# Kernel tuning notes

Hardware: AMD Instinct MI355X
Metric: run time of the kernel (lower is better)

The kernel has to match this reference:

```python
import jax, jax.numpy as jnp
import numpy as np

B = 1024
NUM_DENSE = 13
NUM_SPARSE = 26
VOCAB = 100000
EMB_DIM = 16
BOT = [512, 256, 64, 16]
TOP = [1024, 512, 256]
D_INT = BOT[-1] + NUM_SPARSE * EMB_DIM  # 432
OUT_INT = D_INT * (D_INT + 1) // 2      # 93528


def setup_inputs() -> dict:
    key = jax.random.key(0)
    ks = jax.random.split(key, 32)
    inp = {
        "dense_features": jax.random.normal(ks[0], (B, NUM_DENSE), jnp.float32),
        "sparse_features": jax.random.randint(ks[1], (B, NUM_SPARSE), 0, VOCAB),
        "emb_tables": jax.random.normal(ks[2], (NUM_SPARSE, VOCAB, EMB_DIM), jnp.float32) * 0.02,
    }
    # bottom MLP weights (in, out) convention
    dims = [NUM_DENSE] + BOT
    for i in range(len(BOT)):
        inp[f"bw{i}"] = jax.random.normal(ks[3 + i], (dims[i], dims[i + 1]), jnp.float32) * 0.02
        inp[f"bb{i}"] = jnp.zeros((dims[i + 1],), jnp.float32)
    tdims = [BOT[-1] + OUT_INT] + TOP + [1]
    for i in range(len(TOP) + 1):
        inp[f"tw{i}"] = jax.random.normal(ks[10 + i], (tdims[i], tdims[i + 1]), jnp.float32) * 0.02
        inp[f"tb{i}"] = jnp.zeros((tdims[i + 1],), jnp.float32)
    return inp


def _forward(dense_features, emb_tables, bws, bbs, tws, tbs, sparse_features):
    # bottom MLP: Linear+ReLU stacks
    h = dense_features
    for w, b in zip(bws, bbs):
        h = jax.nn.relu(h @ w + b)
    dense_out = h  # (B, 16)
    # embedding lookups: table t indexed by column t of sparse_features
    # emb_tables: (F, V, E); gather per-table then flatten -> (B, F*E)
    emb = jnp.take_along_axis(
        emb_tables[None],  # (1, F, V, E)
        sparse_features.T[None, :, :, None].transpose(0, 1, 2, 3) * 0 + sparse_features.T[None, :, :, None],
        axis=2,
    )  # placeholder avoided below
    # cleaner: vmap over tables
    emb = jax.vmap(lambda tbl, idx: tbl[idx], in_axes=(0, 1))(emb_tables, sparse_features)  # (F, B, E)
    emb = jnp.transpose(emb, (1, 0, 2)).reshape(dense_features.shape[0], -1)  # (B, F*E)
    x = jnp.concatenate([dense_out, emb], axis=1)  # (B, D_INT)
    # pairwise interaction: upper triangle (incl. diagonal) of outer product.
    iu0, iu1 = np.triu_indices(x.shape[1])
    inter = x[:, iu0] * x[:, iu1]  # (B, OUT_INT) -- only needed entries
    z = jnp.concatenate([dense_out, inter], axis=1)
    n_top = len(tws)
    for i, (w, b) in enumerate(zip(tws, tbs)):
        z = z @ w + b
        if i < n_top - 1:
            z = jax.nn.relu(z)
    return z


def reference(dense_features, sparse_features, emb_tables,
              bw0, bb0, bw1, bb1, bw2, bb2, bw3, bb3,
              tw0, tb0, tw1, tb1, tw2, tb2, tw3, tb3):
    bws = [bw0, bw1, bw2, bw3]
    bbs = [bb0, bb1, bb2, bb3]
    tws = [tw0, tw1, tw2, tw3]
    tbs = [tb0, tb1, tb2, tb3]
    return _forward(dense_features, emb_tables, bws, bbs, tws, tbs, sparse_features)
```

## Files before the change

### kernel.cpp

```cpp
#include <hip/hip_runtime.h>
#include <stdint.h>

typedef unsigned short ushort_t;
typedef __attribute__((ext_vector_type(4))) float f32x4;
typedef __attribute__((ext_vector_type(8))) short s16x8;

#define DEVFN static __device__ __forceinline__

constexpr int B_   = 1024;
constexpr int P_   = 93528;
constexpr int K1   = 93544;
constexpr int Kp   = 94208;
constexpr int SPLITS = 16;
constexpr int KCH  = Kp / SPLITS;
constexpr int KSTEPS = KCH / 64;

DEVFN ushort_t f2bf(float f) {
  union { float f; unsigned int u; } x; x.f = f;
  unsigned int r = x.u + 0x7FFFu + ((x.u >> 16) & 1u);
  return (ushort_t)(r >> 16);
}

DEVFN void gload_lds16(const void* g, void* l) {
  __builtin_amdgcn_global_load_lds((const __attribute__((address_space(1))) unsigned int*)g,
                                   (__attribute__((address_space(3))) unsigned int*)l, 16, 0, 0);
}

__global__ __launch_bounds__(256) void k_pre(const float* __restrict__ dense,
    const int* __restrict__ sparse, const float* __restrict__ tbl,
    const float* __restrict__ bw0, const float* __restrict__ bb0,
    const float* __restrict__ bw1, const float* __restrict__ bb1,
    const float* __restrict__ bw2, const float* __restrict__ bb2,
    const float* __restrict__ bw3, const float* __restrict__ bb3,
    const float* __restrict__ tw0,
    int* __restrict__ iu, float* __restrict__ xT, ushort_t* __restrict__ WT) {
  __shared__ float sm[3392];
  int bid = blockIdx.x, t = threadIdx.x;
  if (bid < 256) {
    float* xs = sm;
    float* h1 = sm + 64;
    float* h2 = h1 + 2048;
    float* h3 = h2 + 1024;
    int m0 = bid * 4;
    if (t < 52) xs[t] = dense[m0 * 13 + t];
    __syncthreads();
    #pragma unroll
    for (int h = 0; h < 2; ++h) {
      int n = h * 256 + t;
      float a[4];
      float bv = bb0[n];
      #pragma unroll
      for (int r = 0; r < 4; ++r) a[r] = bv;
      for (int k = 0; k < 13; ++k) {
        float w = bw0[k * 512 + n];
        #pragma unroll
        for (int r = 0; r < 4; ++r) a[r] = fmaf(xs[r * 13 + k], w, a[r]);
      }
      #pragma unroll
      for (int r = 0; r < 4; ++r) h1[r * 512 + n] = fmaxf(a[r], 0.f);
    }
    __syncthreads();
    {
      int n = t;
      float a[4];
      float bv = bb1[n];
      #pragma unroll
      for (int r = 0; r < 4; ++r) a[r] = bv;
      #pragma unroll 8
      for (int k = 0; k < 512; ++k) {
        float w = bw1[k * 256 + n];
        #pragma unroll
        for (int r = 0; r < 4; ++r) a[r] = fmaf(h1[r * 512 + k], w, a[r]);
      }
      #pragma unroll
      for (int r = 0; r < 4; ++r) h2[r * 256 + n] = fmaxf(a[r], 0.f);
    }
    __syncthreads();
    {
      int n = t & 63, r = t >> 6;
      float a = bb2[n];
      #pragma unroll 8
      for (int k = 0; k < 256; ++k) a = fmaf(h2[r * 256 + k], bw2[k * 64 + n], a);
      h3[r * 64 + n] = fmaxf(a, 0.f);
    }
    __syncthreads();
    if (t < 64) {
      int n = t & 15, r = t >> 4;
      float a = bb3[n];
      #pragma unroll 8
      for (int k = 0; k < 64; ++k) a = fmaf(h3[r * 64 + k], bw3[k * 16 + n], a);
      xT[(size_t)n * B_ + m0 + r] = fmaxf(a, 0.f);
    }
  } else if (bid < 624) {
    int bb = bid - 256;
    int k = bb * 256 + t;
    if (bb < 8) {
      int idx = bb * 256 + t;
      xT[432 * 1024 + idx] = (idx < 1024) ? 1.f : 0.f;
    }
    if (k >= Kp) return;
    int v;
    if (k < 16) v = k | (432 << 16);
    else if (k >= K1) v = 433 | (433 << 16);
    else {
      int p = k - 16;
      float s = sqrtf((float)(748225 - 8 * p));
      int i = (int)((865.0f - s) * 0.5f);
      if (i < 0) i = 0; if (i > 431) i = 431;
      while (i < 431 && (i + 1) * (865 - (i + 1)) / 2 <= p) ++i;
      while (i > 0 && i * (865 - i) / 2 > p) --i;
      int j = i + (p - i * (865 - i) / 2);
      v = i | (j << 16);
    }
    iu[k] = v;
  } else if (bid < 728) {
    int e = bid - 624;
    int f = e >> 2;
    int b = (e & 3) * 256 + t;
    int idx = sparse[(size_t)b * 26 + f];
    const float4* src = (const float4*)(tbl + ((size_t)f * 100000 + idx) * 16);
    #pragma unroll
    for (int q = 0; q < 4; ++q) {
      float4 v = src[q];
      int r = 16 + f * 16 + q * 4;
      xT[(size_t)(r + 0) * B_ + b] = v.x;
      xT[(size_t)(r + 1) * B_ + b] = v.y;
      xT[(size_t)(r + 2) * B_ + b] = v.z;
      xT[(size_t)(r + 3) * B_ + b] = v.w;
    }
  } else {
    int idx = bid - 728;
    int k0 = (idx % 368) * 256, n0 = (idx / 368) * 64;
    int nl = t & 63, kq = t >> 6;
    int n = n0 + nl;
    int kbase = k0 + kq * 64;
    const float* src = tw0 + (size_t)kbase * 1024 + n;
    ushort_t* dst = WT + ((size_t)(kbase >> 3) * 1024 + n) * 8;
    bool full = (kbase + 64 <= K1);
    #pragma unroll
    for (int g = 0; g < 8; ++g) {
      float v[8];
      if (full) {
        #pragma unroll
        for (int e = 0; e < 8; ++e) v[e] = src[(size_t)(g * 8 + e) << 10];
      } else {
        #pragma unroll
        for (int e = 0; e < 8; ++e) {
          int k = kbase + g * 8 + e;
          v[e] = (k < K1) ? src[(size_t)(g * 8 + e) << 10] : 0.f;
        }
      }
      union { uint32_t w4[4]; int4 v4; } o;
      asm("v_cvt_pk_bf16_f32 %0, %1, %2" : "=v"(o.w4[0]) : "v"(v[0]), "v"(v[1]));
      asm("v_cvt_pk_bf16_f32 %0, %1, %2" : "=v"(o.w4[1]) : "v"(v[2]), "v"(v[3]));
      asm("v_cvt_pk_bf16_f32 %0, %1, %2" : "=v"(o.w4[2]) : "v"(v[4]), "v"(v[5]));
      asm("v_cvt_pk_bf16_f32 %0, %1, %2" : "=v"(o.w4[3]) : "v"(v[6]), "v"(v[7]));
      *(int4*)(dst + (size_t)g * 8192) = o.v4;
    }
  }
}

__global__ __launch_bounds__(256, 8) void k_genz(const float* __restrict__ xT,
                                                 const int* __restrict__ iu,
                                                 ushort_t* __restrict__ Z) {
  __shared__ int ls_iu[512];
  int idx = blockIdx.x, t = threadIdx.x;
  int l = t & 63, w = t >> 6;
  int mb = (idx & 15) * 64;
  int kt = (idx >> 4) * 512;
  ls_iu[t] = iu[kt + t];
  ls_iu[256 + t] = iu[kt + 256 + t];
  __syncthreads();
  uint32_t moff = mb + l;
  int kw = w * 128;
  #pragma unroll 2
  for (int g = 0; g < 16; ++g) {
    int kloc = kw + g * 8;
    int4 ij0 = *(const int4*)&ls_iu[kloc];
    int4 ij1 = *(const int4*)&ls_iu[kloc + 4];
    float p[8];
    {
      int v0 = ij0.x, v1 = ij0.y, v2 = ij0.z, v3 = ij0.w;
      p[0] = xT[(uint32_t)((v0 & 0xFFFF) << 10) + moff] * xT[(uint32_t)((v0 >> 16) << 10) + moff];
      p[1] = xT[(uint32_t)((v1 & 0xFFFF) << 10) + moff] * xT[(uint32_t)((v1 >> 16) << 10) + moff];
      p[2] = xT[(uint32_t)((v2 & 0xFFFF) << 10) + moff] * xT[(uint32_t)((v2 >> 16) << 10) + moff];
      p[3] = xT[(uint32_t)((v3 & 0xFFFF) << 10) + moff] * xT[(uint32_t)((v3 >> 16) << 10) + moff];
      v0 = ij1.x; v1 = ij1.y; v2 = ij1.z; v3 = ij1.w;
      p[4] = xT[(uint32_t)((v0 & 0xFFFF) << 10) + moff] * xT[(uint32_t)((v0 >> 16) << 10) + moff];
      p[5] = xT[(uint32_t)((v1 & 0xFFFF) << 10) + moff] * xT[(uint32_t)((v1 >> 16) << 10) + moff];
      p[6] = xT[(uint32_t)((v2 & 0xFFFF) << 10) + moff] * xT[(uint32_t)((v2 >> 16) << 10) + moff];
      p[7] = xT[(uint32_t)((v3 & 0xFFFF) << 10) + moff] * xT[(uint32_t)((v3 >> 16) << 10) + moff];
    }
    union { uint32_t w4[4]; int4 v4; } o;
    asm("v_cvt_pk_bf16_f32 %0, %1, %2" : "=v"(o.w4[0]) : "v"(p[0]), "v"(p[1]));
    asm("v_cvt_pk_bf16_f32 %0, %1, %2" : "=v"(o.w4[1]) : "v"(p[2]), "v"(p[3]));
    asm("v_cvt_pk_bf16_f32 %0, %1, %2" : "=v"(o.w4[2]) : "v"(p[4]), "v"(p[5]));
    asm("v_cvt_pk_bf16_f32 %0, %1, %2" : "=v"(o.w4[3]) : "v"(p[6]), "v"(p[7]));
    int kglob = kt + kloc;
    *(int4*)&Z[((size_t)(kglob >> 3) * 1024 + moff) * 8] = o.v4;
  }
}

__global__ __launch_bounds__(512, 2) void k_gemm(const ushort_t* __restrict__ Z,
                                                 const ushort_t* __restrict__ WT,
                                                 float* __restrict__ part) {
  __shared__ ushort_t lds[65536];
  int t = threadIdx.x;
  int bid = blockIdx.x;
  int x = bid & 7, r = bid >> 3;
  int g = (x << 3) | (r & 7);
  int s = g >> 2;
  int m0 = (g & 3) * 256, n0 = (r >> 3) * 256;
  int kb = s * KCH;

  int rr = t >> 3, cc = t & 7;
  int cs = cc ^ (rr & 7);
  const ushort_t* pa0 = Z  + (((size_t)(kb >> 3) + cs) * 1024 + m0 + rr) * 8;
  const ushort_t* pb0 = WT + (((size_t)(kb >> 3) + cs) * 1024 + n0 + rr) * 8;
  int l0 = t * 8;

  int w = t >> 6, l = t & 63;
  int wm = (w >> 2) * 128, wn = (w & 3) * 64;
  int lhi = l >> 4, llo = l & 15;

  f32x4 acc[8][4];
  #pragma unroll
  for (int a = 0; a < 8; ++a)
    #pragma unroll
    for (int b = 0; b < 4; ++b) acc[a][b] = f32x4{0.f, 0.f, 0.f, 0.f};

  s16x8 bf[4][2], afX[4], afY[4];

  auto rdA = [&](s16x8* dst, int mfb, const ushort_t* Ab) {
    #pragma unroll
    for (int j = 0; j < 2; ++j)
      #pragma unroll
      for (int ks = 0; ks < 2; ++ks) {
        int row = wm + (mfb + j) * 16 + llo;
        int ch = (ks * 4 + lhi) ^ (row & 7);
        dst[j * 2 + ks] = *(const s16x8*)&Ab[row * 64 + ch * 8];
      }
  };
  auto rdB = [&](const ushort_t* Bb) {
    #pragma unroll
    for (int nf = 0; nf < 4; ++nf)
      #pragma unroll
      for (int ks = 0; ks < 2; ++ks) {
        int row = wn + nf * 16 + llo;
        int ch = (ks * 4 + lhi) ^ (row & 7);
        bf[nf][ks] = *(const s16x8*)&Bb[row * 64 + ch * 8];
      }
  };

#define MFMA_PHASE(P, AF)                                                        \
  __builtin_amdgcn_s_barrier();                                                  \
  asm volatile("s_waitcnt lgkmcnt(0)" ::: "memory");                             \
  __builtin_amdgcn_sched_barrier(0);                                             \
  __builtin_amdgcn_s_setprio(1);                                                 \
  _Pragma("unroll")                                                              \
  for (int j = 0; j < 2; ++j)                                                    \
    _Pragma("unroll")                                                            \
    for (int nf = 0; nf < 4; ++nf)                                               \
      _Pragma("unroll")                                                          \
      for (int ks = 0; ks < 2; ++ks)                                             \
        acc[(P) * 2 + j][nf] = __builtin_amdgcn_mfma_f32_16x16x32_bf16(          \
            AF[j * 2 + ks], bf[nf][ks], acc[(P) * 2 + j][nf], 0, 0, 0);          \
  __builtin_amdgcn_s_setprio(0);                                                 \
  __builtin_amdgcn_sched_barrier(0);                                             \
  __builtin_amdgcn_s_barrier();

  #pragma unroll
  for (int i = 0; i < 4; ++i) gload_lds16(pa0 + i * 512, &lds[i * 4096 + l0]);
  #pragma unroll
  for (int i = 0; i < 4; ++i) gload_lds16(pb0 + i * 512, &lds[32768 + i * 4096 + l0]);
  #pragma unroll
  for (int i = 0; i < 4; ++i) gload_lds16(pb0 + 65536 + i * 512, &lds[32768 + 16384 + i * 4096 + l0]);
  asm volatile("s_waitcnt vmcnt(4)" ::: "memory");
  __builtin_amdgcn_s_barrier();
  rdA(afX, 0, &lds[0]);

  for (int tt = 0; tt < KSTEPS; ++tt) {
    const ushort_t* Ab = &lds[(tt & 1) * 16384];
    const ushort_t* An = &lds[((tt + 1) & 1) * 16384];
    const ushort_t* Bb = &lds[32768 + (tt & 1) * 16384];
    ushort_t* dA  = &lds[((tt + 1) & 1) * 16384];
    ushort_t* dB2 = &lds[32768 + (tt & 1) * 16384];
    const ushort_t* sA  = pa0 + (size_t)(tt + 1) * 65536;
    const ushort_t* sB2 = pb0 + (size_t)(tt + 2) * 65536;
    bool pf1 = (tt + 1 < KSTEPS);
    bool pf2 = (tt + 2 < KSTEPS);

    rdB(Bb);
    rdA(afY, 2, Ab);
    if (pf1) {
      gload_lds16(sA,       dA + l0);
      gload_lds16(sA + 512, dA + 4096 + l0);
    }
    MFMA_PHASE(0, afX)

    rdA(afX, 4, Ab);
    if (pf1) {
      gload_lds16(sA + 1024, dA + 2 * 4096 + l0);
      gload_lds16(sA + 1536, dA + 3 * 4096 + l0);
    }
    MFMA_PHASE(1, afY)

    rdA(afY, 6, Ab);
    if (pf2) {
      gload_lds16(sB2,       dB2 + l0);
      gload_lds16(sB2 + 512, dB2 + 4096 + l0);
    }
    MFMA_PHASE(2, afX)

    if (pf1) {
      if (pf2) asm volatile("s_waitcnt vmcnt(2)" ::: "memory");
      else     asm volatile("s_waitcnt vmcnt(0)" ::: "memory");
      rdA(afX, 0, An);
    }
    if (pf2) {
      gload_lds16(sB2 + 1024, dB2 + 2 * 4096 + l0);
      gload_lds16(sB2 + 1536, dB2 + 3 * 4096 + l0);
    }
    MFMA_PHASE(3, afY)
  }
#undef MFMA_PHASE

  float* pbase = part + ((size_t)s << 20);
  #pragma unroll
  for (int mf = 0; mf < 8; ++mf)
    #pragma unroll
    for (int nf = 0; nf < 4; ++nf) {
      int n = n0 + wn + nf * 16 + llo;
      #pragma unroll
      for (int r2 = 0; r2 < 4; ++r2) {
        int m = m0 + wm + mf * 16 + lhi * 4 + r2;
        pbase[(size_t)m * 1024 + n] = acc[mf][nf][r2];
      }
    }
}

__global__ __launch_bounds__(256) void k_red(const float* __restrict__ part,
                                             const float* __restrict__ bias,
                                             float* __restrict__ z1) {
  int idx = blockIdx.x * 256 + threadIdx.x;
  float a = bias[idx & 1023];
  #pragma unroll
  for (int s = 0; s < SPLITS; ++s) a += part[((size_t)s << 20) + idx];
  z1[idx] = fmaxf(a, 0.f);
}

template<int K, int N>
__global__ __launch_bounds__(256) void k_sgemm(const float* __restrict__ A,
                                               const float* __restrict__ W,
                                               const float* __restrict__ bias,
                                               float* __restrict__ C) {
  __shared__ float As[16][34];
  __shared__ float Bs[16][68];
  int t = threadIdx.x;
  int m0 = blockIdx.x * 32, n0 = blockIdx.y * 64;
  int tx = t & 15, ty = t >> 4;
  float acc[2][4];
  #pragma unroll
  for (int j = 0; j < 2; ++j)
    #pragma unroll
    for (int q = 0; q < 4; ++q) acc[j][q] = 0.f;
  int ar = t >> 3, ak = (t & 7) * 2;
  int bk = t >> 4, bn = (t & 15) * 4;
  for (int k0 = 0; k0 < K; k0 += 16) {
    float2 av = *(const float2*)&A[(size_t)(m0 + ar) * K + k0 + ak];
    float4 bv = *(const float4*)&W[(size_t)(k0 + bk) * N + n0 + bn];
    __syncthreads();
    As[ak][ar] = av.x; As[ak + 1][ar] = av.y;
    *(float4*)&Bs[bk][bn] = bv;
    __syncthreads();
    #pragma unroll
    for (int k = 0; k < 16; ++k) {
      float2 a = *(const float2*)&As[k][ty * 2];
      float4 b = *(const float4*)&Bs[k][tx * 4];
      acc[0][0] = fmaf(a.x, b.x, acc[0][0]); acc[0][1] = fmaf(a.x, b.y, acc[0][1]);
      acc[0][2] = fmaf(a.x, b.z, acc[0][2]); acc[0][3] = fmaf(a.x, b.w, acc[0][3]);
      acc[1][0] = fmaf(a.y, b.x, acc[1][0]); acc[1][1] = fmaf(a.y, b.y, acc[1][1]);
      acc[1][2] = fmaf(a.y, b.z, acc[1][2]); acc[1][3] = fmaf(a.y, b.w, acc[1][3]);
    }
  }
  #pragma unroll
  for (int j = 0; j < 2; ++j) {
    int m = m0 + ty * 2 + j;
    float4 o;
    o.x = fmaxf(acc[j][0] + bias[n0 + tx * 4 + 0], 0.f);
    o.y = fmaxf(acc[j][1] + bias[n0 + tx * 4 + 1], 0.f);
    o.z = fmaxf(acc[j][2] + bias[n0 + tx * 4 + 2], 0.f);
    o.w = fmaxf(acc[j][3] + bias[n0 + tx * 4 + 3], 0.f);
    *(float4*)&C[(size_t)m * N + n0 + tx * 4] = o;
  }
}

__global__ __launch_bounds__(256) void k_last(const float* __restrict__ z3,
                                              const float* __restrict__ w,
                                              const float* __restrict__ bias,
                                              float* __restrict__ out) {
  int t = threadIdx.x, l = t & 63, wv = t >> 6;
  int m = blockIdx.x * 4 + wv;
  float s = 0.f;
  #pragma unroll
  for (int c = 0; c < 4; ++c) s = fmaf(z3[(size_t)m * 256 + c * 64 + l], w[c * 64 + l], s);
  #pragma unroll
  for (int off = 32; off; off >>= 1) s += __shfl_down(s, off, 64);
  if (l == 0) out[m] = s + bias[0];
}

__global__ __launch_bounds__(256) void k_z1init(const float* __restrict__ bias, float* __restrict__ z1) {
  int idx = blockIdx.x * 256 + threadIdx.x;
  z1[idx] = bias[idx & 1023];
}
__global__ __launch_bounds__(256) void k_relu(float* __restrict__ z1) {
  int idx = blockIdx.x * 256 + threadIdx.x;
  z1[idx] = fmaxf(z1[idx], 0.f);
}
constexpr int FB_S = 8;
__global__ __launch_bounds__(256) void k_fbgemm(const float* __restrict__ xT,
                                                const int* __restrict__ iu,
                                                const float* __restrict__ tw0,
                                                float* __restrict__ z1) {
  __shared__ float zs[32 * 64];
  __shared__ float wsb[32 * 64];
  int t = threadIdx.x;
  int m0 = blockIdx.x * 64, n0 = blockIdx.y * 64, s = blockIdx.z;
  int kch = (K1 + FB_S - 1) / FB_S;
  int k0 = s * kch, kend = min(k0 + kch, K1);
  float acc[16];
  #pragma unroll
  for (int q = 0; q < 16; ++q) acc[q] = 0.f;
  int mm = t & 63, ng = t >> 6;
  for (int kk = k0; kk < kend; kk += 32) {
    __syncthreads();
    for (int sl = t; sl < 2048; sl += 256) {
      int kloc = sl >> 6, v6 = sl & 63;
      int k = kk + kloc;
      float zv = 0.f, wv = 0.f;
      if (k < kend) {
        int ij = iu[k];
        int i = ij & 0xFFFF, j = ij >> 16;
        zv = xT[(size_t)i * B_ + m0 + v6] * xT[(size_t)j * B_ + m0 + v6];
        wv = tw0[(size_t)k * 1024 + n0 + v6];
      }
      zs[kloc * 64 + v6] = zv;
      wsb[kloc * 64 + v6] = wv;
    }
    __syncthreads();
    #pragma unroll 4
    for (int kloc = 0; kloc < 32; ++kloc) {
      float zv = zs[kloc * 64 + mm];
      #pragma unroll
      for (int q = 0; q < 16; ++q)
        acc[q] = fmaf(zv, wsb[kloc * 64 + ng * 16 + q], acc[q]);
    }
  }
  #pragma unroll
  for (int q = 0; q < 16; ++q)
    atomicAdd(&z1[(size_t)(m0 + mm) * 1024 + n0 + ng * 16 + q], acc[q]);
}

extern "C" void kernel_launch(void* const* d_in, const int* in_sizes, int n_in,
                              void* d_out, int out_size, void* d_ws, size_t ws_size,
                              hipStream_t stream) {
  const float* dense  = (const float*)d_in[0];
  const int*   sparse = (const int*)  d_in[1];
  const float* emb    = (const float*)d_in[2];
  const float* bw0 = (const float*)d_in[3];  const float* bb0 = (const float*)d_in[4];
  const float* bw1 = (const float*)d_in[5];  const float* bb1 = (const float*)d_in[6];
  const float* bw2 = (const float*)d_in[7];  const float* bb2 = (const float*)d_in[8];
  const float* bw3 = (const float*)d_in[9];  const float* bb3 = (const float*)d_in[10];
  const float* tw0 = (const float*)d_in[11]; const float* tb0 = (const float*)d_in[12];
  const float* tw1 = (const float*)d_in[13]; const float* tb1 = (const float*)d_in[14];
  const float* tw2 = (const float*)d_in[15]; const float* tb2 = (const float*)d_in[16];
  const float* tw3 = (const float*)d_in[17]; const float* tb3 = (const float*)d_in[18];
  float* out = (float*)d_out;

  char* ws = (char*)d_ws;
  size_t off = 0;
  auto alloc = [&](size_t bytes) -> char* {
    char* p = ws + off;
    off = (off + bytes + 255) & ~(size_t)255;
    return p;
  };
  float* xT = (float*)alloc((size_t)434 * 1024 * 4);
  int*   iu = (int*)  alloc((size_t)Kp * 4);
  float* z1 = (float*)alloc((size_t)1024 * 1024 * 4);
  float* z2 = (float*)alloc((size_t)1024 * 512 * 4);
  float* z3 = (float*)alloc((size_t)1024 * 256 * 4);
  ushort_t* Z    = (ushort_t*)alloc((size_t)1024 * Kp * 2);
  ushort_t* WT   = (ushort_t*)alloc((size_t)1024 * Kp * 2);
  float*    part = (float*)   alloc((size_t)SPLITS * 1024 * 1024 * 4);
  bool big = (off <= ws_size);

  int preGrid = big ? 6616 : 728;
  k_pre<<<preGrid, 256, 0, stream>>>(dense, sparse, emb, bw0, bb0, bw1, bb1,
                                     bw2, bb2, bw3, bb3, tw0, iu, xT, WT);

  if (big) {
    k_genz<<<2944, 256, 0, stream>>>(xT, iu, Z);
    k_gemm<<<256, 512, 0, stream>>>(Z, WT, part);
    k_red<<<4096, 256, 0, stream>>>(part, tb0, z1);
  } else {
    k_z1init<<<4096, 256, 0, stream>>>(tb0, z1);
    k_fbgemm<<<dim3(16, 16, FB_S), 256, 0, stream>>>(xT, iu, tw0, z1);
    k_relu<<<4096, 256, 0, stream>>>(z1);
  }

  k_sgemm<1024, 512><<<dim3(32, 8), 256, 0, stream>>>(z1, tw1, tb1, z2);
  k_sgemm<512, 256><<<dim3(32, 4), 256, 0, stream>>>(z2, tw2, tb2, z3);
  k_last<<<256, 256, 0, stream>>>(z3, tw3, tb3, out);
}
```

Measured before the change: 479.2 us.

## Fuse weight bf16 conversion into Z generation kernel and reschedule GEMM A-fragment read

Moves the tw0 fp32-to-bf16 packing out of the preprocessing kernel and interleaves it with interaction generation in a new combined kernel, with blocks alternating 2:1 between Z work and weight work. This lets the gather-heavy Z generation overlap with the streaming weight conversion. The weight conversion now reads float4 columns so each thread packs four output columns per k-group. In the GEMM loop, the next A-fragment LDS read is moved after the last MFMA cluster instead of before it, so that cluster can start sooner. Interleaving blocks of different character and the reordered LDS read could change occupancy and latency hiding.

```diff
diff --git a/kernel.cpp b/kernel.cpp
--- a/kernel.cpp
+++ b/kernel.cpp
@@ -32,8 +32,7 @@
     const float* __restrict__ bw1, const float* __restrict__ bb1,
     const float* __restrict__ bw2, const float* __restrict__ bb2,
     const float* __restrict__ bw3, const float* __restrict__ bb3,
-    const float* __restrict__ tw0,
-    int* __restrict__ iu, float* __restrict__ xT, ushort_t* __restrict__ WT) {
+    int* __restrict__ iu, float* __restrict__ xT) {
   __shared__ float sm[3392];
   int bid = blockIdx.x, t = threadIdx.x;
   if (bid < 256) {
@@ -113,7 +112,7 @@
       v = i | (j << 16);
     }
     iu[k] = v;
-  } else if (bid < 728) {
+  } else {
     int e = bid - 624;
     int f = e >> 2;
     int b = (e & 3) * 256 + t;
@@ -128,76 +127,94 @@
       xT[(size_t)(r + 2) * B_ + b] = v.z;
       xT[(size_t)(r + 3) * B_ + b] = v.w;
     }
+  }
+}
+
+__global__ __launch_bounds__(256, 8) void k_gz(const float* __restrict__ xT,
+                                               const int* __restrict__ iu,
+                                               const float* __restrict__ tw0,
+                                               ushort_t* __restrict__ Z,
+                                               ushort_t* __restrict__ WT) {
+  __shared__ int ls_iu[512];
+  int bid = blockIdx.x, t = threadIdx.x;
+  int r3 = bid % 3;
+  if (r3 < 2) {
+    int idx = (bid / 3) * 2 + r3;
+    int l = t & 63, w = t >> 6;
+    int mb = (idx & 15) * 64;
+    int kt = (idx >> 4) * 512;
+    ls_iu[t] = iu[kt + t];
+    ls_iu[256 + t] = iu[kt + 256 + t];
+    __syncthreads();
+    uint32_t moff = mb + l;
+    int kw = w * 128;
+    #pragma unroll 2
+    for (int g = 0; g < 16; ++g) {
+      int kloc = kw + g * 8;
+      int4 ij0 = *(const int4*)&ls_iu[kloc];
+      int4 ij1 = *(const int4*)&ls_iu[kloc + 4];
+      float p[8];
+      {
+        int v0 = ij0.x, v1 = ij0.y, v2 = ij0.z, v3 = ij0.w;
+        p[0] = xT[(uint32_t)((v0 & 0xFFFF) << 10) + moff] * xT[(uint32_t)((v0 >> 16) << 10) + moff];
+        p[1] = xT[(uint32_t)((v1 & 0xFFFF) << 10) + moff] * xT[(uint32_t)((v1 >> 16) << 10) + moff];
+        p[2] = xT[(uint32_t)((v2 & 0xFFFF) << 10) + moff] * xT[(uint32_t)((v2 >> 16) << 10) + moff];
+        p[3] = xT[(uint32_t)((v3 & 0xFFFF) << 10) + moff] * xT[(uint32_t)((v3 >> 16) << 10) + moff];
+        v0 = ij1.x; v1 = ij1.y; v2 = ij1.z; v3 = ij1.w;
+        p[4] = xT[(uint32_t)((v0 & 0xFFFF) << 10) + moff] * xT[(uint32_t)((v0 >> 16) << 10) + moff];
+        p[5] = xT[(uint32_t)((v1 & 0xFFFF) << 10) + moff] * xT[(uint32_t)((v1 >> 16) << 10) + moff];
+        p[6] = xT[(uint32_t)((v2 & 0xFFFF) << 10) + moff] * xT[(uint32_t)((v2 >> 16) << 10) + moff];
+        p[7] = xT[(uint32_t)((v3 & 0xFFFF) << 10) + moff] * xT[(uint32_t)((v3 >> 16) << 10) + moff];
+      }
+      union { uint32_t w4[4]; int4 v4; } o;
+      asm("v_cvt_pk_bf16_f32 %0, %1, %2" : "=v"(o.w4[0]) : "v"(p[0]), "v"(p[1]));
+      asm("v_cvt_pk_bf16_f32 %0, %1, %2" : "=v"(o.w4[1]) : "v"(p[2]), "v"(p[3]));
+      asm("v_cvt_pk_bf16_f32 %0, %1, %2" : "=v"(o.w4[2]) : "v"(p[4]), "v"(p[5]));
+      asm("v_cvt_pk_bf16_f32 %0, %1, %2" : "=v"(o.w4[3]) : "v"(p[6]), "v"(p[7]));
+      int kglob = kt + kloc;
+      *(int4*)&Z[((size_t)(kglob >> 3) * 1024 + moff) * 8] = o.v4;
+    }
   } else {
-    int idx = bid - 728;
-    int k0 = (idx % 368) * 256, n0 = (idx / 368) * 64;
-    int nl = t & 63, kq = t >> 6;
-    int n = n0 + nl;
-    int kbase = k0 + kq * 64;
-    const float* src = tw0 + (size_t)kbase * 1024 + n;
-    ushort_t* dst = WT + ((size_t)(kbase >> 3) * 1024 + n) * 8;
-    bool full = (kbase + 64 <= K1);
+    int idx = bid / 3;
+    int k0 = (idx % 368) * 256, n0 = (idx / 368) * 256;
+    int lane = t & 63, kq = t >> 6;
+    int nb = n0 + lane * 4;
+    int kb0 = k0 + kq * 64;
+    const float* src = tw0 + (size_t)kb0 * 1024 + nb;
     #pragma unroll
     for (int g = 0; g < 8; ++g) {
-      float v[8];
-      if (full) {
+      int kg = kb0 + g * 8;
+      float4 v[8];
+      if (kg + 8 <= K1) {
         #pragma unroll
-        for (int e = 0; e < 8; ++e) v[e] = src[(size_t)(g * 8 + e) << 10];
+        for (int e = 0; e < 8; ++e) v[e] = *(const float4*)&src[(size_t)(g * 8 + e) << 10];
       } else {
         #pragma unroll
         for (int e = 0; e < 8; ++e) {
-          int k = kbase + g * 8 + e;
-          v[e] = (k < K1) ? src[(size_t)(g * 8 + e) << 10] : 0.f;
+          int k = kg + e;
+          v[e] = (k < K1) ? *(const float4*)&src[(size_t)(g * 8 + e) << 10]
+                          : make_float4(0.f, 0.f, 0.f, 0.f);
         }
       }
-      union { uint32_t w4[4]; int4 v4; } o;
-      asm("v_cvt_pk_bf16_f32 %0, %1, %2" : "=v"(o.w4[0]) : "v"(v[0]), "v"(v[1]));
-      asm("v_cvt_pk_bf16_f32 %0, %1, %2" : "=v"(o.w4[1]) : "v"(v[2]), "v"(v[3]));
-      asm("v_cvt_pk_bf16_f32 %0, %1, %2" : "=v"(o.w4[2]) : "v"(v[4]), "v"(v[5]));
-      asm("v_cvt_pk_bf16_f32 %0, %1, %2" : "=v"(o.w4[3]) : "v"(v[6]), "v"(v[7]));
-      *(int4*)(dst + (size_t)g * 8192) = o.v4;
-    }
-  }
-}
-
-__global__ __launch_bounds__(256, 8) void k_genz(const float* __restrict__ xT,
-                                                 const int* __restrict__ iu,
-                                                 ushort_t* __restrict__ Z) {
-  __shared__ int ls_iu[512];
-  int idx = blockIdx.x, t = threadIdx.x;
-  int l = t & 63, w = t >> 6;
-  int mb = (idx & 15) * 64;
-  int kt = (idx >> 4) * 512;
-  ls_iu[t] = iu[kt + t];
-  ls_iu[256 + t] = iu[kt + 256 + t];
-  __syncthreads();
-  uint32_t moff = mb + l;
-  int kw = w * 128;
-  #pragma unroll 2
-  for (int g = 0; g < 16; ++g) {
-    int kloc = kw + g * 8;
-    int4 ij0 = *(const int4*)&ls_iu[kloc];
-    int4 ij1 = *(const int4*)&ls_iu[kloc + 4];
-    float p[8];
-    {
-      int v0 = ij0.x, v1 = ij0.y, v2 = ij0.z, v3 = ij0.w;
-      p[0] = xT[(uint32_t)((v0 & 0xFFFF) << 10) + moff] * xT[(uint32_t)((v0 >> 16) << 10) + moff];
-      p[1] = xT[(uint32_t)((v1 & 0xFFFF) << 10) + moff] * xT[(uint32_t)((v1 >> 16) << 10) + moff];
-      p[2] = xT[(uint32_t)((v2 & 0xFFFF) << 10) + moff] * xT[(uint32_t)((v2 >> 16) << 10) + moff];
-      p[3] = xT[(uint32_t)((v3 & 0xFFFF) << 10) + moff] * xT[(uint32_t)((v3 >> 16) << 10) + moff];
-      v0 = ij1.x; v1 = ij1.y; v2 = ij1.z; v3 = ij1.w;
-      p[4] = xT[(uint32_t)((v0 & 0xFFFF) << 10) + moff] * xT[(uint32_t)((v0 >> 16) << 10) + moff];
-      p[5] = xT[(uint32_t)((v1 & 0xFFFF) << 10) + moff] * xT[(uint32_t)((v1 >> 16) << 10) + moff];
-      p[6] = xT[(uint32_t)((v2 & 0xFFFF) << 10) + moff] * xT[(uint32_t)((v2 >> 16) << 10) + moff];
-      p[7] = xT[(uint32_t)((v3 & 0xFFFF) << 10) + moff] * xT[(uint32_t)((v3 >> 16) << 10) + moff];
-    }
-    union { uint32_t w4[4]; int4 v4; } o;
-    asm("v_cvt_pk_bf16_f32 %0, %1, %2" : "=v"(o.w4[0]) : "v"(p[0]), "v"(p[1]));
-    asm("v_cvt_pk_bf16_f32 %0, %1, %2" : "=v"(o.w4[1]) : "v"(p[2]), "v"(p[3]));
-    asm("v_cvt_pk_bf16_f32 %0, %1, %2" : "=v"(o.w4[2]) : "v"(p[4]), "v"(p[5]));
-    asm("v_cvt_pk_bf16_f32 %0, %1, %2" : "=v"(o.w4[3]) : "v"(p[6]), "v"(p[7]));
-    int kglob = kt + kloc;
-    *(int4*)&Z[((size_t)(kglob >> 3) * 1024 + moff) * 8] = o.v4;
+      ushort_t* dst = WT + ((size_t)(kg >> 3) * 1024 + nb) * 8;
+      #pragma unroll
+      for (int j = 0; j < 4; ++j) {
+        float e0 = (j == 0) ? v[0].x : (j == 1) ? v[0].y : (j == 2) ? v[0].z : v[0].w;
+        float e1 = (j == 0) ? v[1].x : (j == 1) ? v[1].y : (j == 2) ? v[1].z : v[1].w;
+        float e2 = (j == 0) ? v[2].x : (j == 1) ? v[2].y : (j == 2) ? v[2].z : v[2].w;
+        float e3 = (j == 0) ? v[3].x : (j == 1) ? v[3].y : (j == 2) ? v[3].z : v[3].w;
+        float e4 = (j == 0) ? v[4].x : (j == 1) ? v[4].y : (j == 2) ? v[4].z : v[4].w;
+        float e5 = (j == 0) ? v[5].x : (j == 1) ? v[5].y : (j == 2) ? v[5].z : v[5].w;
+        float e6 = (j == 0) ? v[6].x : (j == 1) ? v[6].y : (j == 2) ? v[6].z : v[6].w;
+        float e7 = (j == 0) ? v[7].x : (j == 1) ? v[7].y : (j == 2) ? v[7].z : v[7].w;
+        union { uint32_t w4[4]; int4 v4; } o;
+        asm("v_cvt_pk_bf16_f32 %0, %1, %2" : "=v"(o.w4[0]) : "v"(e0), "v"(e1));
+        asm("v_cvt_pk_bf16_f32 %0, %1, %2" : "=v"(o.w4[1]) : "v"(e2), "v"(e3));
+        asm("v_cvt_pk_bf16_f32 %0, %1, %2" : "=v"(o.w4[2]) : "v"(e4), "v"(e5));
+        asm("v_cvt_pk_bf16_f32 %0, %1, %2" : "=v"(o.w4[3]) : "v"(e6), "v"(e7));
+        *(int4*)(dst + (size_t)j * 8) = o.v4;
+      }
+    }
   }
 }
 
@@ -252,8 +269,7 @@
       }
   };
 
-#define MFMA_PHASE(P, AF)                                                        \
-  __builtin_amdgcn_s_barrier();                                                  \
+#define MFMA_CLUSTER(P, AF)                                                      \
   asm volatile("s_waitcnt lgkmcnt(0)" ::: "memory");                             \
   __builtin_amdgcn_sched_barrier(0);                                             \
   __builtin_amdgcn_s_setprio(1);                                                 \
@@ -266,7 +282,11 @@
         acc[(P) * 2 + j][nf] = __builtin_amdgcn_mfma_f32_16x16x32_bf16(          \
             AF[j * 2 + ks], bf[nf][ks], acc[(P) * 2 + j][nf], 0, 0, 0);          \
   __builtin_amdgcn_s_setprio(0);                                                 \
-  __builtin_amdgcn_sched_barrier(0);                                             \
+  __builtin_amdgcn_sched_barrier(0);
+
+#define MFMA_PHASE(P, AF)                                                        \
+  __builtin_amdgcn_s_barrier();                                                  \
+  MFMA_CLUSTER(P, AF)                                                            \
   __builtin_amdgcn_s_barrier();
 
   #pragma unroll
@@ -315,15 +335,18 @@
     if (pf1) {
       if (pf2) asm volatile("s_waitcnt vmcnt(2)" ::: "memory");
       else     asm volatile("s_waitcnt vmcnt(0)" ::: "memory");
-      rdA(afX, 0, An);
     }
     if (pf2) {
       gload_lds16(sB2 + 1024, dB2 + 2 * 4096 + l0);
       gload_lds16(sB2 + 1536, dB2 + 3 * 4096 + l0);
     }
-    MFMA_PHASE(3, afY)
+    __builtin_amdgcn_s_barrier();
+    MFMA_CLUSTER(3, afY)
+    if (pf1) rdA(afX, 0, An);
+    __builtin_amdgcn_s_barrier();
   }
 #undef MFMA_PHASE
+#undef MFMA_CLUSTER
 
   float* pbase = part + ((size_t)s << 20);
   #pragma unroll
@@ -494,12 +517,11 @@
   float*    part = (float*)   alloc((size_t)SPLITS * 1024 * 1024 * 4);
   bool big = (off <= ws_size);
 
-  int preGrid = big ? 6616 : 728;
-  k_pre<<<preGrid, 256, 0, stream>>>(dense, sparse, emb, bw0, bb0, bw1, bb1,
-                                     bw2, bb2, bw3, bb3, tw0, iu, xT, WT);
+  k_pre<<<728, 256, 0, stream>>>(dense, sparse, emb, bw0, bb0, bw1, bb1,
+                                 bw2, bb2, bw3, bb3, iu, xT);
 
   if (big) {
-    k_genz<<<2944, 256, 0, stream>>>(xT, iu, Z);
+    k_gz<<<4416, 256, 0, stream>>>(xT, iu, tw0, Z, WT);
     k_gemm<<<256, 512, 0, stream>>>(Z, WT, part);
     k_red<<<4096, 256, 0, stream>>>(part, tb0, z1);
   } else {
```

New measurement: 546.2 us. 1.14x slower.
